# Optimization experiments

Hardware: AMD Instinct MI355X
Metric: run time of the kernel (lower is better)

Reference implementation:

```python
import jax, jax.numpy as jnp
import numpy as np
from jax import lax

EPS = 1e-12  # F.normalize default eps


def _l2_normalize(v, axis=-1):
    n = jnp.linalg.norm(v, axis=axis, keepdims=True)
    return v / jnp.maximum(n, EPS)


def setup_inputs() -> dict:
    key = jax.random.key(0)
    k1, k2, k3 = jax.random.split(key, 3)
    x = jax.random.normal(k1, (4, 768, 4096), dtype=jnp.float32)
    conv_w = jax.random.normal(k2, (128, 768, 3), dtype=jnp.float32) * 0.02
    codebook = jax.random.normal(k3, (8192, 128), dtype=jnp.float32)
    return {"x": x, "conv_w": conv_w, "codebook": codebook}


def reference(x, conv_w, codebook):
    # in_proj: Conv1d(input_dim -> codebook_dim, k=3, stride=2, pad=1, no bias)
    x_e = lax.conv_general_dilated(
        x, conv_w,
        window_strides=(2,), padding=[(1, 1)],
        dimension_numbers=("NCH", "OIH", "NCH"),
    )  # [b, d, t]
    b, d, t = x_e.shape
    enc = _l2_normalize(x_e.transpose(0, 2, 1).reshape(b * t, d))  # [(b t), d]
    cb = _l2_normalize(codebook)                                    # [K, d]
    # dist = ||e||^2 - 2 e.c + ||c||^2
    dist = (
        jnp.sum(enc * enc, axis=1, keepdims=True)
        - 2.0 * enc @ cb.T
        + jnp.sum(cb * cb, axis=1)[None, :]
    )  # [(b t), K]
    indices = jnp.argmax(-dist, axis=1).reshape(b, t)
    return indices
```

## Files before the change

### kernel.cpp

```cpp
#include <hip/hip_runtime.h>

#define EPS 1e-12f

#define BATCH 4
#define CIN   768
#define LIN   4096
#define DCODE 128
#define TOUT  2048
#define NROWS (BATCH*TOUT)
#define KCB   8192
#define KCONV 2304

#define OFF_CN2  0u
#define OFF_BS   32768u
#define OFF_BI   163840u
#define OFF_EH   294912u
#define OFF_EL   2392064u
#define OFF_CH   4489216u
#define OFF_CL   6586368u
#define OFF_WHT  8683520u
#define OFF_WLT  9273344u
#define OFF_PART 9863168u
#define OFF_XTH  18251776u
#define OFF_XTL  43417600u

typedef _Float16 half_t;
typedef __attribute__((ext_vector_type(8))) _Float16 half8;
typedef __attribute__((ext_vector_type(2))) _Float16 half2v;
typedef __attribute__((ext_vector_type(4))) float f32x4;

__global__ __launch_bounds__(256) void k_wt2(const float* __restrict__ w,
                                             half_t* __restrict__ wht,
                                             half_t* __restrict__ wlt) {
    int k = blockIdx.x * 256 + threadIdx.x;
    int n = blockIdx.y;
    if (k >= KCONV) return;
    int j = (k >= 1536) ? 2 : (k >= 768) ? 1 : 0;
    int c = k - j * 768;
    float v = w[(size_t)n * KCONV + c * 3 + j];
    half_t h = (half_t)v;
    wht[(size_t)n * KCONV + k] = h;
    wlt[(size_t)n * KCONV + k] = (half_t)(v - (float)h);
}

__global__ __launch_bounds__(256) void k_xt(const float* __restrict__ x,
                                            half_t* __restrict__ xth,
                                            half_t* __restrict__ xtl) {
    __shared__ float tile[32][33];
    const int s0 = blockIdx.x * 32;
    const int c0 = blockIdx.y * 32;
    const int b  = blockIdx.z;
    const int sl = threadIdx.x & 31;
    const int cl = threadIdx.x >> 5;
    const float* xg = x + ((size_t)b * CIN + c0) * LIN + s0;
    #pragma unroll
    for (int p = 0; p < 4; ++p) {
        int c = cl + p * 8;
        tile[c][sl] = xg[(size_t)c * LIN + sl];
    }
    __syncthreads();
    const int wcc = (threadIdx.x & 15) * 2;
    const int wss = threadIdx.x >> 4;
    #pragma unroll
    for (int p = 0; p < 2; ++p) {
        int s = wss + p * 16;
        float v0 = tile[wcc][s], v1 = tile[wcc + 1][s];
        half_t h0 = (half_t)v0, h1 = (half_t)v1;
        half_t l0 = (half_t)(v0 - (float)h0), l1 = (half_t)(v1 - (float)h1);
        size_t o = ((size_t)b * LIN + s0 + s) * CIN + c0 + wcc;
        *(half2v*)(xth + o) = half2v{h0, h1};
        *(half2v*)(xtl + o) = half2v{l0, l1};
    }
}

__global__ __launch_bounds__(256) void k_cbnorm(const float* __restrict__ cb,
                                                half_t* __restrict__ ch,
                                                half_t* __restrict__ cl,
                                                float* __restrict__ cn2) {
    int wid  = threadIdx.x >> 6;
    int lane = threadIdx.x & 63;
    int k = blockIdx.x * 4 + wid;
    const float2* src = (const float2*)cb + (size_t)k * 64;
    float2 v = src[lane];
    float ss = v.x * v.x + v.y * v.y;
    #pragma unroll
    for (int m = 1; m < 64; m <<= 1) ss += __shfl_xor(ss, m);
    float inv = 1.0f / fmaxf(sqrtf(ss), EPS);
    float nx = v.x * inv, ny = v.y * inv;
    half_t hx = (half_t)nx, hy = (half_t)ny;
    half_t lx = (half_t)(nx - (float)hx), ly = (half_t)(ny - (float)hy);
    ((half2v*)ch)[(size_t)k * 64 + lane] = half2v{hx, hy};
    ((half2v*)cl)[(size_t)k * 64 + lane] = half2v{lx, ly};
    if (lane == 0) cn2[k] = ss * inv * inv;
}

__global__ __launch_bounds__(256, 1) void k_conv_mfma(
        const half_t* __restrict__ xth, const half_t* __restrict__ xtl,
        const half_t* __restrict__ wht, const half_t* __restrict__ wlt,
        float* __restrict__ part) {
    extern __shared__ char smem[];
    const int tid  = threadIdx.x;
    const int lane = tid & 63;
    const int w    = tid >> 6;
    const int wr   = w >> 1;
    const int wc   = w & 1;
    const int lr   = lane & 15;
    const int lg   = lane >> 4;
    const int r0   = blockIdx.x * 64;
    const int ks   = blockIdx.y;
    const int b    = r0 >> 11;
    const int t00  = r0 & 2047;
    const int kbase = ks * 1152;

    const half_t* msrc = (w >> 1) ? wlt : wht;
    auto stage = [&](int t, int buf) {
        int k0 = kbase + t * 128;
        #pragma unroll
        for (int i = 0; i < 16; ++i) {
            int col_l = (w & 1) * 64 + i * 4 + lg;
            int ksrc  = (lr * 16) ^ ((col_l & 7) << 4);
            const char* g = (const char*)msrc + (size_t)col_l * 4608
                          + (size_t)k0 * 2 + ksrc;
            char* l = smem + buf * 65536 + w * 16384 + i * 1024;
            __builtin_amdgcn_global_load_lds(
                (const __attribute__((address_space(1))) void*)(uintptr_t)g,
                (__attribute__((address_space(3))) void*)(uintptr_t)l, 16, 0, 0);
        }
    };

    f32x4 acc[2][4];
    #pragma unroll
    for (int g = 0; g < 2; ++g)
        #pragma unroll
        for (int cg = 0; cg < 4; ++cg) acc[g][cg] = f32x4{0.f, 0.f, 0.f, 0.f};

    stage(0, 0);
    __syncthreads();

    int buf = 0;
    for (int t = 0; t < 9; ++t) {
        int k0 = kbase + t * 128;
        int j  = (k0 >= 1536) ? 2 : (k0 >= 768) ? 1 : 0;
        int c0 = k0 - j * 768;
        half8 ah[2][4], al[2][4];
        #pragma unroll
        for (int g = 0; g < 2; ++g) {
            int trow = t00 + wr * 32 + g * 16 + lr;
            int s = 2 * trow - 1 + j;
            bool valid = (unsigned)s < (unsigned)LIN;
            size_t o = ((size_t)b * LIN + (valid ? s : 0)) * CIN + c0 + lg * 8;
            const half8* ph = (const half8*)(xth + o);
            const half8* pl = (const half8*)(xtl + o);
            #pragma unroll
            for (int kc = 0; kc < 4; ++kc) {
                half8 vh = {}, vl = {};
                if (valid) { vh = ph[kc * 4]; vl = pl[kc * 4]; }
                ah[g][kc] = vh; al[g][kc] = vl;
            }
        }
        if (t < 8) stage(t + 1, buf ^ 1);
        const char* bhp = smem + buf * 65536;
        const char* blp = bhp + 32768;
        #pragma unroll 2
        for (int cg = 0; cg < 4; ++cg) {
            int col   = wc * 64 + cg * 16 + lr;
            int kswz  = (col & 7) << 4;
            int cbyte = col * 256;
            half8 bhf[4], blf[4];
            #pragma unroll
            for (int kc = 0; kc < 4; ++kc) {
                int kb = (kc * 64 + lg * 16) ^ kswz;
                bhf[kc] = *(const half8*)(bhp + cbyte + kb);
                blf[kc] = *(const half8*)(blp + cbyte + kb);
            }
            #pragma unroll
            for (int kc = 0; kc < 4; ++kc) {
                #pragma unroll
                for (int g = 0; g < 2; ++g) {
                    acc[g][cg] = __builtin_amdgcn_mfma_f32_16x16x32_f16(ah[g][kc], bhf[kc], acc[g][cg], 0, 0, 0);
                    acc[g][cg] = __builtin_amdgcn_mfma_f32_16x16x32_f16(al[g][kc], bhf[kc], acc[g][cg], 0, 0, 0);
                    acc[g][cg] = __builtin_amdgcn_mfma_f32_16x16x32_f16(ah[g][kc], blf[kc], acc[g][cg], 0, 0, 0);
                }
            }
        }
        __syncthreads();
        buf ^= 1;
    }

    float* pb = part + (size_t)ks * NROWS * DCODE;
    #pragma unroll
    for (int g = 0; g < 2; ++g)
        #pragma unroll
        for (int cg = 0; cg < 4; ++cg) {
            int col = wc * 64 + cg * 16 + lr;
            #pragma unroll
            for (int rr = 0; rr < 4; ++rr) {
                int row = r0 + wr * 32 + g * 16 + lg * 4 + rr;
                pb[(size_t)row * DCODE + col] = acc[g][cg][rr];
            }
        }
}

__global__ __launch_bounds__(256) void k_encnorm(const float* __restrict__ part,
                                                 half_t* __restrict__ eh,
                                                 half_t* __restrict__ el) {
    int wid  = threadIdx.x >> 6;
    int lane = threadIdx.x & 63;
    int r = blockIdx.x * 4 + wid;
    const float2* p0 = (const float2*)part + (size_t)r * 64;
    const float2* p1 = (const float2*)(part + (size_t)NROWS * DCODE) + (size_t)r * 64;
    float2 a = p0[lane];
    float2 c = p1[lane];
    a.x += c.x; a.y += c.y;
    float ss = a.x * a.x + a.y * a.y;
    #pragma unroll
    for (int m = 1; m < 64; m <<= 1) ss += __shfl_xor(ss, m);
    float inv = 1.0f / fmaxf(sqrtf(ss), EPS);
    float nx = a.x * inv, ny = a.y * inv;
    half_t hx = (half_t)nx, hy = (half_t)ny;
    half_t lx = (half_t)(nx - (float)hx), ly = (half_t)(ny - (float)hy);
    ((half2v*)eh)[(size_t)r * 64 + lane] = half2v{hx, hy};
    ((half2v*)el)[(size_t)r * 64 + lane] = half2v{lx, ly};
}

__global__ __launch_bounds__(256, 1) void k_dist(const half_t* __restrict__ eh,
                                                 const half_t* __restrict__ el,
                                                 const half_t* __restrict__ ch,
                                                 const half_t* __restrict__ cl,
                                                 const float* __restrict__ cn2,
                                                 float* __restrict__ best_s,
                                                 int* __restrict__ best_i) {
    extern __shared__ char smem[];
    const int tid  = threadIdx.x;
    const int lane = tid & 63;
    const int w    = tid >> 6;
    const int lr   = lane & 15;
    const int lg   = lane >> 4;
    const int r0   = blockIdx.x * 128;
    const int kqbase = blockIdx.y * 2048;

    half8 ah[2][4], al[2][4];
    #pragma unroll
    for (int g = 0; g < 2; ++g) {
        int row = r0 + w * 32 + g * 16 + lr;
        const half8* ph = (const half8*)(eh + (size_t)row * 128 + lg * 8);
        const half8* pl = (const half8*)(el + (size_t)row * 128 + lg * 8);
        #pragma unroll
        for (int kc = 0; kc < 4; ++kc) { ah[g][kc] = ph[kc * 4]; al[g][kc] = pl[kc * 4]; }
    }

    const half_t* msrc = (w >> 1) ? cl : ch;
    auto stage = [&](int t, int buf) {
        #pragma unroll
        for (int i = 0; i < 16; ++i) {
            int col_l = (w & 1) * 64 + i * 4 + lg;
            int ksrc  = (lr * 16) ^ ((col_l & 7) << 4);
            const char* g = (const char*)msrc
                          + ((size_t)(kqbase + t * 128 + col_l)) * 256 + ksrc;
            char* l = smem + buf * 65536 + w * 16384 + i * 1024;
            __builtin_amdgcn_global_load_lds(
                (const __attribute__((address_space(1))) void*)(uintptr_t)g,
                (__attribute__((address_space(3))) void*)(uintptr_t)l, 16, 0, 0);
        }
    };

    float bs[2][4]; int bi[2][4];
    #pragma unroll
    for (int g = 0; g < 2; ++g)
        #pragma unroll
        for (int r = 0; r < 4; ++r) { bs[g][r] = -3.4e38f; bi[g][r] = 0; }

    stage(0, 0);
    __syncthreads();

    int buf = 0;
    for (int t = 0; t < 16; ++t) {
        if (t < 15) stage(t + 1, buf ^ 1);
        float cnv[8];
        #pragma unroll
        for (int cg = 0; cg < 8; ++cg)
            cnv[cg] = cn2[kqbase + t * 128 + cg * 16 + lr];
        const char* bhp = smem + buf * 65536;
        const char* blp = bhp + 32768;
        #pragma unroll 2
        for (int cg = 0; cg < 8; ++cg) {
            int col   = cg * 16 + lr;
            int kswz  = (col & 7) << 4;
            int cbyte = col * 256;
            half8 bhf[4], blf[4];
            #pragma unroll
            for (int kc = 0; kc < 4; ++kc) {
                int kb = (kc * 64 + lg * 16) ^ kswz;
                bhf[kc] = *(const half8*)(bhp + cbyte + kb);
                blf[kc] = *(const half8*)(blp + cbyte + kb);
            }
            f32x4 acc[2] = {f32x4{0.f,0.f,0.f,0.f}, f32x4{0.f,0.f,0.f,0.f}};
            #pragma unroll
            for (int kc = 0; kc < 4; ++kc) {
                #pragma unroll
                for (int g = 0; g < 2; ++g) {
                    acc[g] = __builtin_amdgcn_mfma_f32_16x16x32_f16(ah[g][kc], bhf[kc], acc[g], 0, 0, 0);
                    acc[g] = __builtin_amdgcn_mfma_f32_16x16x32_f16(al[g][kc], bhf[kc], acc[g], 0, 0, 0);
                    acc[g] = __builtin_amdgcn_mfma_f32_16x16x32_f16(ah[g][kc], blf[kc], acc[g], 0, 0, 0);
                }
            }
            int n = kqbase + t * 128 + cg * 16 + lr;
            #pragma unroll
            for (int g = 0; g < 2; ++g)
                #pragma unroll
                for (int r = 0; r < 4; ++r) {
                    float sc = 2.0f * acc[g][r] - cnv[cg];
                    if (sc > bs[g][r]) { bs[g][r] = sc; bi[g][r] = n; }
                }
        }
        __syncthreads();
        buf ^= 1;
    }

    #pragma unroll
    for (int g = 0; g < 2; ++g)
        #pragma unroll
        for (int r = 0; r < 4; ++r) {
            float s = bs[g][r]; int i = bi[g][r];
            #pragma unroll
            for (int m = 1; m < 16; m <<= 1) {
                float os = __shfl_xor(s, m);
                int   oi = __shfl_xor(i, m);
                if (os > s || (os == s && oi < i)) { s = os; i = oi; }
            }
            if (lr == 0) {
                int row = r0 + w * 32 + g * 16 + lg * 4 + r;
                best_s[(size_t)blockIdx.y * NROWS + row] = s;
                best_i[(size_t)blockIdx.y * NROWS + row] = i;
            }
        }
}

__global__ __launch_bounds__(256) void k_merge(const float* __restrict__ bs,
                                               const int* __restrict__ bi,
                                               int* __restrict__ out) {
    int r = blockIdx.x * 256 + threadIdx.x;
    if (r >= NROWS) return;
    float s = bs[r]; int i = bi[r];
    #pragma unroll
    for (int q = 1; q < 4; ++q) {
        float s2 = bs[(size_t)q * NROWS + r];
        int   i2 = bi[(size_t)q * NROWS + r];
        if (s2 > s || (s2 == s && i2 < i)) { s = s2; i = i2; }
    }
    out[r] = i;
}

extern "C" void kernel_launch(void* const* d_in, const int* in_sizes, int n_in,
                              void* d_out, int out_size, void* d_ws, size_t ws_size,
                              hipStream_t stream) {
    const float* x  = (const float*)d_in[0];
    const float* w  = (const float*)d_in[1];
    const float* cb = (const float*)d_in[2];
    char* ws = (char*)d_ws;
    float*  cn2  = (float*)(ws + OFF_CN2);
    float*  bs   = (float*)(ws + OFF_BS);
    int*    bi   = (int*)(ws + OFF_BI);
    half_t* eh   = (half_t*)(ws + OFF_EH);
    half_t* el   = (half_t*)(ws + OFF_EL);
    half_t* chh  = (half_t*)(ws + OFF_CH);
    half_t* cll  = (half_t*)(ws + OFF_CL);
    half_t* wht  = (half_t*)(ws + OFF_WHT);
    half_t* wlt  = (half_t*)(ws + OFF_WLT);
    float*  part = (float*)(ws + OFF_PART);
    half_t* xth  = (half_t*)(ws + OFF_XTH);
    half_t* xtl  = (half_t*)(ws + OFF_XTL);
    int*    out  = (int*)d_out;

    hipFuncSetAttribute((const void*)k_dist,
                        hipFuncAttributeMaxDynamicSharedMemorySize, 131072);
    hipFuncSetAttribute((const void*)k_conv_mfma,
                        hipFuncAttributeMaxDynamicSharedMemorySize, 131072);

    k_wt2     <<<dim3(9, 128), 256, 0, stream>>>(w, wht, wlt);
    k_cbnorm  <<<2048, 256, 0, stream>>>(cb, chh, cll, cn2);
    k_xt      <<<dim3(128, 24, 4), 256, 0, stream>>>(x, xth, xtl);
    k_conv_mfma<<<dim3(128, 2), 256, 131072, stream>>>(xth, xtl, wht, wlt, part);
    k_encnorm <<<2048, 256, 0, stream>>>(part, eh, el);
    k_dist    <<<dim3(64, 4), 256, 131072, stream>>>(eh, el, chh, cll, cn2, bs, bi);
    k_merge   <<<32, 256, 0, stream>>>(bs, bi, out);
}
```

Measured before the change: 206.9 us.

## Retile distance kernel so waves split codebook columns, reorder conv MFMA loops

In k_dist, each block now handles 64 rows, and each wave takes a separate 32-column slice of every 128-codebook tile instead of a separate slice of rows. Each wave keeps all 64 rows of A fragments in registers, and an LDS cross-wave argmax reduction runs at the end. The grid becomes 128x2, with 4096 codes per block, so k_merge combines two partials instead of four. In the conv kernel, the MFMA loop is reordered to iterate kc outermost and issue independent accumulator chains back to back, which aims to hide MFMA dependency latency. The new layout raises register pressure (4x4 A fragments plus 16 best-score registers) and cuts LDS reads per MFMA, at the cost of an extra reduction and barrier.

```diff
diff --git a/kernel.cpp b/kernel.cpp
--- a/kernel.cpp
+++ b/kernel.cpp
@@ -161,27 +161,33 @@
         if (t < 8) stage(t + 1, buf ^ 1);
         const char* bhp = smem + buf * 65536;
         const char* blp = bhp + 32768;
-        #pragma unroll 2
-        for (int cg = 0; cg < 4; ++cg) {
-            int col   = wc * 64 + cg * 16 + lr;
-            int kswz  = (col & 7) << 4;
-            int cbyte = col * 256;
+        #pragma unroll
+        for (int kc = 0; kc < 4; ++kc) {
             half8 bhf[4], blf[4];
             #pragma unroll
-            for (int kc = 0; kc < 4; ++kc) {
-                int kb = (kc * 64 + lg * 16) ^ kswz;
-                bhf[kc] = *(const half8*)(bhp + cbyte + kb);
-                blf[kc] = *(const half8*)(blp + cbyte + kb);
-            }
-            #pragma unroll
-            for (int kc = 0; kc < 4; ++kc) {
-                #pragma unroll
-                for (int g = 0; g < 2; ++g) {
-                    acc[g][cg] = __builtin_amdgcn_mfma_f32_16x16x32_f16(ah[g][kc], bhf[kc], acc[g][cg], 0, 0, 0);
-                    acc[g][cg] = __builtin_amdgcn_mfma_f32_16x16x32_f16(al[g][kc], bhf[kc], acc[g][cg], 0, 0, 0);
-                    acc[g][cg] = __builtin_amdgcn_mfma_f32_16x16x32_f16(ah[g][kc], blf[kc], acc[g][cg], 0, 0, 0);
-                }
-            }
+            for (int cg = 0; cg < 4; ++cg) {
+                int col   = wc * 64 + cg * 16 + lr;
+                int kswz  = (col & 7) << 4;
+                int cbyte = col * 256;
+                int kb    = (kc * 64 + lg * 16) ^ kswz;
+                bhf[cg] = *(const half8*)(bhp + cbyte + kb);
+                blf[cg] = *(const half8*)(blp + cbyte + kb);
+            }
+            #pragma unroll
+            for (int cg = 0; cg < 4; ++cg)
+                #pragma unroll
+                for (int g = 0; g < 2; ++g)
+                    acc[g][cg] = __builtin_amdgcn_mfma_f32_16x16x32_f16(ah[g][kc], bhf[cg], acc[g][cg], 0, 0, 0);
+            #pragma unroll
+            for (int cg = 0; cg < 4; ++cg)
+                #pragma unroll
+                for (int g = 0; g < 2; ++g)
+                    acc[g][cg] = __builtin_amdgcn_mfma_f32_16x16x32_f16(al[g][kc], bhf[cg], acc[g][cg], 0, 0, 0);
+            #pragma unroll
+            for (int cg = 0; cg < 4; ++cg)
+                #pragma unroll
+                for (int g = 0; g < 2; ++g)
+                    acc[g][cg] = __builtin_amdgcn_mfma_f32_16x16x32_f16(ah[g][kc], blf[cg], acc[g][cg], 0, 0, 0);
         }
         __syncthreads();
         buf ^= 1;
@@ -236,13 +242,13 @@
     const int w    = tid >> 6;
     const int lr   = lane & 15;
     const int lg   = lane >> 4;
-    const int r0   = blockIdx.x * 128;
-    const int kqbase = blockIdx.y * 2048;
-
-    half8 ah[2][4], al[2][4];
-    #pragma unroll
-    for (int g = 0; g < 2; ++g) {
-        int row = r0 + w * 32 + g * 16 + lr;
+    const int r0   = blockIdx.x * 64;
+    const int kqbase = blockIdx.y * 4096;
+
+    half8 ah[4][4], al[4][4];
+    #pragma unroll
+    for (int g = 0; g < 4; ++g) {
+        int row = r0 + g * 16 + lr;
         const half8* ph = (const half8*)(eh + (size_t)row * 128 + lg * 8);
         const half8* pl = (const half8*)(el + (size_t)row * 128 + lg * 8);
         #pragma unroll
@@ -264,64 +270,79 @@
         }
     };
 
-    float bs[2][4]; int bi[2][4];
-    #pragma unroll
-    for (int g = 0; g < 2; ++g)
-        #pragma unroll
-        for (int r = 0; r < 4; ++r) { bs[g][r] = -3.4e38f; bi[g][r] = 0; }
+    float bs[4][4]; int bi[4][4];
+    #pragma unroll
+    for (int g = 0; g < 4; ++g)
+        #pragma unroll
+        for (int rr = 0; rr < 4; ++rr) { bs[g][rr] = -3.4e38f; bi[g][rr] = 0; }
 
     stage(0, 0);
     __syncthreads();
 
     int buf = 0;
-    for (int t = 0; t < 16; ++t) {
-        if (t < 15) stage(t + 1, buf ^ 1);
-        float cnv[8];
-        #pragma unroll
-        for (int cg = 0; cg < 8; ++cg)
-            cnv[cg] = cn2[kqbase + t * 128 + cg * 16 + lr];
+    for (int t = 0; t < 32; ++t) {
+        if (t < 31) stage(t + 1, buf ^ 1);
+        float cnv[2];
+        #pragma unroll
+        for (int cg = 0; cg < 2; ++cg)
+            cnv[cg] = cn2[kqbase + t * 128 + w * 32 + cg * 16 + lr];
         const char* bhp = smem + buf * 65536;
         const char* blp = bhp + 32768;
-        #pragma unroll 2
-        for (int cg = 0; cg < 8; ++cg) {
-            int col   = cg * 16 + lr;
-            int kswz  = (col & 7) << 4;
-            int cbyte = col * 256;
-            half8 bhf[4], blf[4];
-            #pragma unroll
-            for (int kc = 0; kc < 4; ++kc) {
-                int kb = (kc * 64 + lg * 16) ^ kswz;
-                bhf[kc] = *(const half8*)(bhp + cbyte + kb);
-                blf[kc] = *(const half8*)(blp + cbyte + kb);
-            }
-            f32x4 acc[2] = {f32x4{0.f,0.f,0.f,0.f}, f32x4{0.f,0.f,0.f,0.f}};
-            #pragma unroll
-            for (int kc = 0; kc < 4; ++kc) {
-                #pragma unroll
-                for (int g = 0; g < 2; ++g) {
-                    acc[g] = __builtin_amdgcn_mfma_f32_16x16x32_f16(ah[g][kc], bhf[kc], acc[g], 0, 0, 0);
-                    acc[g] = __builtin_amdgcn_mfma_f32_16x16x32_f16(al[g][kc], bhf[kc], acc[g], 0, 0, 0);
-                    acc[g] = __builtin_amdgcn_mfma_f32_16x16x32_f16(ah[g][kc], blf[kc], acc[g], 0, 0, 0);
+        f32x4 acc[4][2];
+        #pragma unroll
+        for (int g = 0; g < 4; ++g)
+            #pragma unroll
+            for (int cg = 0; cg < 2; ++cg) acc[g][cg] = f32x4{0.f, 0.f, 0.f, 0.f};
+        #pragma unroll
+        for (int kc = 0; kc < 4; ++kc) {
+            half8 bhf[2], blf[2];
+            #pragma unroll
+            for (int cg = 0; cg < 2; ++cg) {
+                int col   = w * 32 + cg * 16 + lr;
+                int kswz  = (col & 7) << 4;
+                int cbyte = col * 256;
+                int kb    = (kc * 64 + lg * 16) ^ kswz;
+                bhf[cg] = *(const half8*)(bhp + cbyte + kb);
+                blf[cg] = *(const half8*)(blp + cbyte + kb);
+            }
+            #pragma unroll
+            for (int cg = 0; cg < 2; ++cg)
+                #pragma unroll
+                for (int g = 0; g < 4; ++g)
+                    acc[g][cg] = __builtin_amdgcn_mfma_f32_16x16x32_f16(ah[g][kc], bhf[cg], acc[g][cg], 0, 0, 0);
+            #pragma unroll
+            for (int cg = 0; cg < 2; ++cg)
+                #pragma unroll
+                for (int g = 0; g < 4; ++g)
+                    acc[g][cg] = __builtin_amdgcn_mfma_f32_16x16x32_f16(al[g][kc], bhf[cg], acc[g][cg], 0, 0, 0);
+            #pragma unroll
+            for (int cg = 0; cg < 2; ++cg)
+                #pragma unroll
+                for (int g = 0; g < 4; ++g)
+                    acc[g][cg] = __builtin_amdgcn_mfma_f32_16x16x32_f16(ah[g][kc], blf[cg], acc[g][cg], 0, 0, 0);
+        }
+        #pragma unroll
+        for (int g = 0; g < 4; ++g)
+            #pragma unroll
+            for (int cg = 0; cg < 2; ++cg) {
+                int n = kqbase + t * 128 + w * 32 + cg * 16 + lr;
+                #pragma unroll
+                for (int rr = 0; rr < 4; ++rr) {
+                    float sc = 2.0f * acc[g][cg][rr] - cnv[cg];
+                    if (sc > bs[g][rr]) { bs[g][rr] = sc; bi[g][rr] = n; }
                 }
             }
-            int n = kqbase + t * 128 + cg * 16 + lr;
-            #pragma unroll
-            for (int g = 0; g < 2; ++g)
-                #pragma unroll
-                for (int r = 0; r < 4; ++r) {
-                    float sc = 2.0f * acc[g][r] - cnv[cg];
-                    if (sc > bs[g][r]) { bs[g][r] = sc; bi[g][r] = n; }
-                }
-        }
         __syncthreads();
         buf ^= 1;
     }
 
-    #pragma unroll
-    for (int g = 0; g < 2; ++g)
-        #pragma unroll
-        for (int r = 0; r < 4; ++r) {
-            float s = bs[g][r]; int i = bi[g][r];
+    float* redS = (float*)smem;
+    int*   redI = (int*)(smem + 1024);
+    #pragma unroll
+    for (int g = 0; g < 4; ++g)
+        #pragma unroll
+        for (int rr = 0; rr < 4; ++rr) {
+            float s = bs[g][rr]; int i = bi[g][rr];
             #pragma unroll
             for (int m = 1; m < 16; m <<= 1) {
                 float os = __shfl_xor(s, m);
@@ -329,11 +350,23 @@
                 if (os > s || (os == s && oi < i)) { s = os; i = oi; }
             }
             if (lr == 0) {
-                int row = r0 + w * 32 + g * 16 + lg * 4 + r;
-                best_s[(size_t)blockIdx.y * NROWS + row] = s;
-                best_i[(size_t)blockIdx.y * NROWS + row] = i;
-            }
-        }
+                int row = g * 16 + lg * 4 + rr;
+                redS[w * 64 + row] = s;
+                redI[w * 64 + row] = i;
+            }
+        }
+    __syncthreads();
+    if (tid < 64) {
+        float s = redS[tid]; int i = redI[tid];
+        #pragma unroll
+        for (int w2 = 1; w2 < 4; ++w2) {
+            float s2 = redS[w2 * 64 + tid];
+            int   i2 = redI[w2 * 64 + tid];
+            if (s2 > s || (s2 == s && i2 < i)) { s = s2; i = i2; }
+        }
+        best_s[(size_t)blockIdx.y * NROWS + r0 + tid] = s;
+        best_i[(size_t)blockIdx.y * NROWS + r0 + tid] = i;
+    }
 }
 
 __global__ __launch_bounds__(256) void k_merge(const float* __restrict__ bs,
@@ -343,7 +376,7 @@
     if (r >= NROWS) return;
     float s = bs[r]; int i = bi[r];
     #pragma unroll
-    for (int q = 1; q < 4; ++q) {
+    for (int q = 1; q < 2; ++q) {
         float s2 = bs[(size_t)q * NROWS + r];
         int   i2 = bi[(size_t)q * NROWS + r];
         if (s2 > s || (s2 == s && i2 < i)) { s = s2; i = i2; }
@@ -382,6 +415,6 @@
     k_xt      <<<dim3(128, 24, 4), 256, 0, stream>>>(x, xth, xtl);
     k_conv_mfma<<<dim3(128, 2), 256, 131072, stream>>>(xth, xtl, wht, wlt, part);
     k_encnorm <<<2048, 256, 0, stream>>>(part, eh, el);
-    k_dist    <<<dim3(64, 4), 256, 131072, stream>>>(eh, el, chh, cll, cn2, bs, bi);
+    k_dist    <<<dim3(128, 2), 256, 131072, stream>>>(eh, el, chh, cll, cn2, bs, bi);
     k_merge   <<<32, 256, 0, stream>>>(bs, bi, out);
 }
```

Result: no change. 204.2 us (-1.3%).
